# Performance work log

Hardware: AMD Instinct MI355X
Metric: run time of the kernel (lower is better)

Reference implementation:

```python
import jax, jax.numpy as jnp
import numpy as np

N_NODES = 100000


def gcn_conv(x, W, b, src, dst, n):
    """PyG GCNConv: add self-loops, symmetric normalization, aggregate."""
    x = x @ W  # [N, out]
    loop = jnp.arange(n, dtype=src.dtype)
    src_f = jnp.concatenate([src, loop])  # sources (message origins)
    dst_f = jnp.concatenate([dst, loop])  # targets (aggregation index)
    ones = jnp.ones(src_f.shape[0], dtype=x.dtype)
    deg = jax.ops.segment_sum(ones, dst_f, num_segments=n)
    dinv = jnp.where(deg > 0, jax.lax.rsqrt(deg), 0.0)
    norm = dinv[src_f] * dinv[dst_f]  # [E+N]
    msg = x[src_f] * norm[:, None]  # gather + scale
    out = jax.ops.segment_sum(msg, dst_f, num_segments=n)  # scatter-add
    return out + b


def setup_inputs() -> dict:
    key = jax.random.key(0)
    k1, k2, k3, k4 = jax.random.split(key, 4)
    in_f, hid, ncls = 128, 128, 64
    n_edges = 1600000
    x = jax.random.normal(k1, (N_NODES, in_f), dtype=jnp.float32)
    W1 = jax.random.normal(k2, (in_f, hid), dtype=jnp.float32) * (1.0 / np.sqrt(in_f))
    b1 = jnp.zeros((hid,), dtype=jnp.float32)
    W2 = jax.random.normal(k3, (hid, ncls), dtype=jnp.float32) * (1.0 / np.sqrt(hid))
    b2 = jnp.zeros((ncls,), dtype=jnp.float32)
    edge_index = jax.random.randint(k4, (2, n_edges), 0, N_NODES, dtype=jnp.int32)
    return {"x": x, "W1": W1, "b1": b1, "W2": W2, "b2": b2, "edge_index": edge_index}


def reference(x, W1, b1, W2, b2, edge_index):
    src, dst = edge_index[0], edge_index[1]
    n = x.shape[0]
    h = gcn_conv(x, W1, b1, src, dst, n)
    h = jax.nn.relu(h)
    # dropout p=0.5 is identity in eval mode
    h = gcn_conv(h, W2, b2, src, dst, n)
    return jax.nn.log_softmax(h, axis=1)
```

## Files before the change

kernel.cpp:

```cpp
#include <hip/hip_runtime.h>
#include <math.h>

#define N_NODES 100000
#define N_EDGES 1600000
#define NB 391
#define MROWS 100096
#define CH 3200

typedef __attribute__((ext_vector_type(8))) short short8;
typedef __attribute__((ext_vector_type(4))) float f32x4;
typedef __attribute__((ext_vector_type(2))) float f32x2;

__device__ __forceinline__ short f2b(float f) {
    unsigned u = __float_as_uint(f);
    unsigned r = (u + 0x7FFFu + ((u >> 16) & 1u)) >> 16;
    return (short)r;
}
__device__ __forceinline__ unsigned pk2(float a, float b) {
    return (unsigned)(unsigned short)f2b(a) | ((unsigned)(unsigned short)f2b(b) << 16);
}
__device__ __forceinline__ unsigned char f2q(float v) {
    return (unsigned char)(__builtin_amdgcn_cvt_pk_fp8_f32(v, 0.f, 0, false) & 0xFF);
}
__device__ __forceinline__ void acc2(f32x2* a, unsigned u) {
    a[0] += __builtin_amdgcn_cvt_pk_f32_fp8((int)u, false);
    a[1] += __builtin_amdgcn_cvt_pk_f32_fp8((int)u, true);
}
__device__ __forceinline__ void acc16(f32x2* a, uint4 u) {
    acc2(a + 0, u.x); acc2(a + 2, u.y); acc2(a + 4, u.z); acc2(a + 6, u.w);
}

__device__ __forceinline__ short8 pack8t(const float* __restrict__ p) {
    float4 v0 = ((const float4*)p)[0];
    float4 v1 = ((const float4*)p)[1];
    union { unsigned u[4]; short8 s; } r;
    r.u[0] = __builtin_amdgcn_perm(__float_as_uint(v0.y), __float_as_uint(v0.x), 0x07060302u);
    r.u[1] = __builtin_amdgcn_perm(__float_as_uint(v0.w), __float_as_uint(v0.z), 0x07060302u);
    r.u[2] = __builtin_amdgcn_perm(__float_as_uint(v1.y), __float_as_uint(v1.x), 0x07060302u);
    r.u[3] = __builtin_amdgcn_perm(__float_as_uint(v1.w), __float_as_uint(v1.z), 0x07060302u);
    return r.s;
}

__global__ __launch_bounds__(512) void init_misc(int* __restrict__ bcnt) {
    int t = threadIdx.x;
    if (t < NB) bcnt[t] = 0;
}

__global__ __launch_bounds__(256) void bucket_count(const int* __restrict__ dst,
                                                    int* __restrict__ bcnt) {
    __shared__ int h[NB];
    int t = threadIdx.x;
    for (int i = t; i < NB; i += 256) h[i] = 0;
    __syncthreads();
    for (int e = blockIdx.x * 256 + t; e < N_EDGES; e += gridDim.x * 256)
        atomicAdd(&h[dst[e] >> 8], 1);
    __syncthreads();
    for (int i = t; i < NB; i += 256)
        if (h[i]) atomicAdd(&bcnt[i], h[i]);
}

__global__ __launch_bounds__(512) void bucket_scan(const int* __restrict__ bcnt,
                                                   int* __restrict__ boffs,
                                                   int* __restrict__ bcur) {
    __shared__ int s[512];
    int t = threadIdx.x;
    int v = (t < NB) ? bcnt[t] : 0;
    s[t] = v;
    __syncthreads();
    for (int off = 1; off < 512; off <<= 1) {
        int u = (t >= off) ? s[t - off] : 0;
        __syncthreads();
        s[t] += u;
        __syncthreads();
    }
    if (t < NB) {
        int ex = s[t] - v;
        boffs[t] = ex;
        bcur[t] = ex;
    }
    if (t == 0) boffs[NB] = N_EDGES;
}

__global__ __launch_bounds__(256) void bucket_scatter(const int* __restrict__ src,
                                                      const int* __restrict__ dst,
                                                      int* __restrict__ bcur,
                                                      unsigned* __restrict__ pairs) {
    __shared__ unsigned lw[CH];
    __shared__ short lb[CH];
    __shared__ int cnt[NB];
    __shared__ int lstart[NB];
    int t = threadIdx.x;
    int e0 = blockIdx.x * CH;
    int n = min(CH, N_EDGES - e0);
    for (int i = t; i < NB; i += 256) cnt[i] = 0;
    __syncthreads();
    for (int i = t; i < n; i += 256) {
        int s = src[e0 + i], d = dst[e0 + i];
        lw[i] = ((unsigned)(d & 255) << 24) | (unsigned)s;
        int b = d >> 8;
        lb[i] = (short)b;
        atomicAdd(&cnt[b], 1);
    }
    __syncthreads();
    for (int b = t; b < NB; b += 256) {
        int c = cnt[b];
        lstart[b] = c ? atomicAdd(&bcur[b], c) : 0;
        cnt[b] = 0;
    }
    __syncthreads();
    for (int i = t; i < n; i += 256) {
        int b = lb[i];
        int lo = atomicAdd(&cnt[b], 1);
        pairs[lstart[b] + lo] = lw[i];
    }
}

__global__ __launch_bounds__(256) void csr_fill_bucket(const unsigned* __restrict__ pairs,
                                                       const int* __restrict__ boffs,
                                                       int2* __restrict__ rinfo,
                                                       float* __restrict__ dinv,
                                                       int* __restrict__ srcs) {
    __shared__ int lcnt[256];
    __shared__ int ls[256];
    int t = threadIdx.x, b = blockIdx.x, base = b << 8;
    lcnt[t] = 0;
    __syncthreads();
    int lo_e = boffs[b], hi_e = boffs[b + 1];
    for (int i = lo_e + t; i < hi_e; i += 256)
        atomicAdd(&lcnt[pairs[i] >> 24], 1);
    __syncthreads();
    int c = lcnt[t];
    int len = c + 1;
    ls[t] = len;
    __syncthreads();
    for (int off = 1; off < 256; off <<= 1) {
        int u = (t >= off) ? ls[t - off] : 0;
        __syncthreads();
        ls[t] += u;
        __syncthreads();
    }
    int rp = lo_e + base + ls[t] - len;
    int node = base + t;
    if (node < N_NODES) {
        rinfo[node] = make_int2(rp, rp + len);
        dinv[node] = rsqrtf((float)len);
        srcs[rp] = node;
    }
    __syncthreads();
    lcnt[t] = rp + 1;
    __syncthreads();
    for (int i = lo_e + t; i < hi_e; i += 256) {
        unsigned p = pairs[i];
        int li = p >> 24;
        int pos = atomicAdd(&lcnt[li], 1);
        srcs[pos] = (int)(p & 0xFFFFFFu);
    }
}

__global__ __launch_bounds__(256) void convert_w(const float* __restrict__ W1,
                                                 const float* __restrict__ W2,
                                                 short* __restrict__ w1h,
                                                 short* __restrict__ w2h) {
    int id = blockIdx.x * 256 + threadIdx.x;
    if (id < 128 * 128) {
        int n = id >> 7, k = id & 127;
        w1h[id] = f2b(W1[k * 128 + n]);
    } else if (id < 128 * 128 + 64 * 128) {
        int j = id - 128 * 128;
        int n = j >> 7, k = j & 127;
        w2h[j] = f2b(W2[k * 64 + n]);
    }
}

__global__ __launch_bounds__(512) void gemm1_mfma(const float* __restrict__ X,
                                                  const short* __restrict__ Wt,
                                                  const float* __restrict__ dinv,
                                                  unsigned char* __restrict__ Yf) {
    __shared__ short Ws[128 * 128];
    const int t = threadIdx.x;
    for (int i = t * 8; i < 128 * 128; i += 512 * 8)
        *(short8*)(Ws + i) = *(const short8*)(Wt + i);
    __syncthreads();

    const int w = t >> 6, lane = t & 63;
    const int m = lane & 15, q = lane >> 4;
    const int r0 = blockIdx.x * 128 + w * 16;
    const int ra = min(r0 + m, N_NODES - 1);

    f32x4 acc[8];
#pragma unroll
    for (int c = 0; c < 8; ++c) acc[c] = (f32x4)(0.f);

#pragma unroll
    for (int kk = 0; kk < 4; ++kk) {
        const int koff = kk * 32 + q * 8;
        short8 a = pack8t(X + (size_t)ra * 128 + koff);
#pragma unroll
        for (int c = 0; c < 8; ++c) {
            short8 bh = *(const short8*)(Ws + (c * 16 + m) * 128 + koff);
            acc[c] = __builtin_amdgcn_mfma_f32_16x16x32_bf16(a, bh, acc[c], 0, 0, 0);
        }
    }

    const int rb0 = r0 + q * 4;
    f32x4 dv = *(const f32x4*)(dinv + rb0);
#pragma unroll
    for (int c = 0; c < 8; ++c) {
        const int col = c * 16 + m;
#pragma unroll
        for (int r = 0; r < 4; ++r) {
            int row = rb0 + r;
            if (row < N_NODES) Yf[(size_t)row * 128 + col] = f2q(acc[c][r] * dv[r]);
        }
    }
}

__global__ __launch_bounds__(512) void gemm2_mfma(const short* __restrict__ H,
                                                  const short* __restrict__ Wt,
                                                  const float* __restrict__ dinv,
                                                  unsigned char* __restrict__ Yf) {
    __shared__ short Ws[64 * 128];
    const int t = threadIdx.x;
    for (int i = t * 8; i < 64 * 128; i += 512 * 8)
        *(short8*)(Ws + i) = *(const short8*)(Wt + i);
    __syncthreads();

    const int w = t >> 6, lane = t & 63;
    const int m = lane & 15, q = lane >> 4;
    const int r0 = blockIdx.x * 128 + w * 16;

    f32x4 acc[4];
#pragma unroll
    for (int c = 0; c < 4; ++c) acc[c] = (f32x4)(0.f);

#pragma unroll
    for (int kk = 0; kk < 4; ++kk) {
        const int koff = kk * 32 + q * 8;
        short8 a = *(const short8*)(H + (size_t)(r0 + m) * 128 + koff);
#pragma unroll
        for (int c = 0; c < 4; ++c) {
            short8 bh = *(const short8*)(Ws + (c * 16 + m) * 128 + koff);
            acc[c] = __builtin_amdgcn_mfma_f32_16x16x32_bf16(a, bh, acc[c], 0, 0, 0);
        }
    }

    const int rb0 = r0 + q * 4;
    f32x4 dv = *(const f32x4*)(dinv + rb0);
#pragma unroll
    for (int c = 0; c < 4; ++c) {
        const int col = c * 16 + m;
#pragma unroll
        for (int r = 0; r < 4; ++r) {
            int row = rb0 + r;
            if (row < N_NODES) Yf[(size_t)row * 64 + col] = f2q(acc[c][r] * dv[r]);
        }
    }
}

__global__ __launch_bounds__(256) void agg_relu(const int2* __restrict__ rinfo,
                                                const int* __restrict__ srcs,
                                                const unsigned char* __restrict__ Yf,
                                                const float* __restrict__ dinv,
                                                const float* __restrict__ b,
                                                short* __restrict__ Hb) {
    int t = threadIdx.x;
    int lane = t & 63, w = t >> 6;
    int g = lane >> 3, fl = lane & 7;
    int node = blockIdx.x * 32 + w * 8 + g;
    const unsigned fo = (unsigned)(fl << 4);
    int2 r = rinfo[node];
    int e = r.x, len = r.y - r.x;
    int mx = len;
    mx = max(mx, __shfl_xor(mx, 8));
    mx = max(mx, __shfl_xor(mx, 16));
    mx = max(mx, __shfl_xor(mx, 32));
    f32x2 a[8];
#pragma unroll
    for (int i = 0; i < 8; ++i) a[i] = (f32x2)(0.f);

    uint4 GA0, GA1;
    unsigned sB0 = 0, sB1 = 0;
    {
        unsigned s0 = (unsigned)srcs[e];
        GA0 = *(const uint4*)(Yf + ((s0 << 7) + fo));
        if (1 < len) {
            unsigned s1 = (unsigned)srcs[e + 1];
            GA1 = *(const uint4*)(Yf + ((s1 << 7) + fo));
        }
        if (2 < len) sB0 = (unsigned)srcs[e + 2];
        if (3 < len) sB1 = (unsigned)srcs[e + 3];
    }
    for (int i = 0; i < mx; i += 2) {
        uint4 GB0, GB1;
        if (i + 2 < len) GB0 = *(const uint4*)(Yf + ((sB0 << 7) + fo));
        if (i + 3 < len) GB1 = *(const uint4*)(Yf + ((sB1 << 7) + fo));
        unsigned sC0 = sB0, sC1 = sB1;
        if (i + 4 < len) sC0 = (unsigned)srcs[e + i + 4];
        if (i + 5 < len) sC1 = (unsigned)srcs[e + i + 5];
        if (i < len)     acc16(a, GA0);
        if (i + 1 < len) acc16(a, GA1);
        GA0 = GB0; GA1 = GB1; sB0 = sC0; sB1 = sC1;
    }

    float sc = dinv[node];
    const float4* bf = (const float4*)b;
    float bb[16];
    *(float4*)(bb + 0)  = bf[fl * 4 + 0];
    *(float4*)(bb + 4)  = bf[fl * 4 + 1];
    *(float4*)(bb + 8)  = bf[fl * 4 + 2];
    *(float4*)(bb + 12) = bf[fl * 4 + 3];
    unsigned u[8];
#pragma unroll
    for (int k = 0; k < 8; ++k) {
        float v0 = fmaxf(sc * a[k][0] + bb[2 * k], 0.f);
        float v1 = fmaxf(sc * a[k][1] + bb[2 * k + 1], 0.f);
        u[k] = pk2(v0, v1);
    }
    uint4* hp = (uint4*)Hb + (size_t)node * 16 + fl * 2;
    hp[0] = make_uint4(u[0], u[1], u[2], u[3]);
    hp[1] = make_uint4(u[4], u[5], u[6], u[7]);
}

__global__ __launch_bounds__(256) void agg_lsm(const int2* __restrict__ rinfo,
                                               const int* __restrict__ srcs,
                                               const unsigned char* __restrict__ Yf,
                                               const float* __restrict__ dinv,
                                               const float* __restrict__ b,
                                               float* __restrict__ out) {
    int t = threadIdx.x;
    int lane = t & 63, w = t >> 6;
    int g = lane >> 2, fl = lane & 3;
    int node = blockIdx.x * 64 + w * 16 + g;
    int nd = min(node, N_NODES - 1);
    const unsigned fo = (unsigned)(fl << 4);
    int2 r = rinfo[nd];
    int e = r.x, len = r.y - r.x;
    int mx = len;
    mx = max(mx, __shfl_xor(mx, 4));
    mx = max(mx, __shfl_xor(mx, 8));
    mx = max(mx, __shfl_xor(mx, 16));
    mx = max(mx, __shfl_xor(mx, 32));
    f32x2 a[8];
#pragma unroll
    for (int i = 0; i < 8; ++i) a[i] = (f32x2)(0.f);

    uint4 GA0, GA1;
    unsigned sB0 = 0, sB1 = 0;
    {
        unsigned s0 = (unsigned)srcs[e];
        GA0 = *(const uint4*)(Yf + ((s0 << 6) + fo));
        if (1 < len) {
            unsigned s1 = (unsigned)srcs[e + 1];
            GA1 = *(const uint4*)(Yf + ((s1 << 6) + fo));
        }
        if (2 < len) sB0 = (unsigned)srcs[e + 2];
        if (3 < len) sB1 = (unsigned)srcs[e + 3];
    }
    for (int i = 0; i < mx; i += 2) {
        uint4 GB0, GB1;
        if (i + 2 < len) GB0 = *(const uint4*)(Yf + ((sB0 << 6) + fo));
        if (i + 3 < len) GB1 = *(const uint4*)(Yf + ((sB1 << 6) + fo));
        unsigned sC0 = sB0, sC1 = sB1;
        if (i + 4 < len) sC0 = (unsigned)srcs[e + i + 4];
        if (i + 5 < len) sC1 = (unsigned)srcs[e + i + 5];
        if (i < len)     acc16(a, GA0);
        if (i + 1 < len) acc16(a, GA1);
        GA0 = GB0; GA1 = GB1; sB0 = sC0; sB1 = sC1;
    }

    float sc = dinv[nd];
    const float4* bf = (const float4*)b;
    float bb[16];
    *(float4*)(bb + 0)  = bf[fl * 4 + 0];
    *(float4*)(bb + 4)  = bf[fl * 4 + 1];
    *(float4*)(bb + 8)  = bf[fl * 4 + 2];
    *(float4*)(bb + 12) = bf[fl * 4 + 3];
    float v[16];
#pragma unroll
    for (int j = 0; j < 16; ++j) v[j] = sc * a[j >> 1][j & 1] + bb[j];
    float m = v[0];
#pragma unroll
    for (int j = 1; j < 16; ++j) m = fmaxf(m, v[j]);
    m = fmaxf(m, __shfl_xor(m, 1));
    m = fmaxf(m, __shfl_xor(m, 2));
    float su = 0.f;
#pragma unroll
    for (int j = 0; j < 16; ++j) su += __expf(v[j] - m);
    su += __shfl_xor(su, 1);
    su += __shfl_xor(su, 2);
    float ls = m + logf(su);
    if (node < N_NODES) {
        float4* op = (float4*)out + (size_t)node * 16 + fl * 4;
        op[0] = make_float4(v[0] - ls,  v[1] - ls,  v[2] - ls,  v[3] - ls);
        op[1] = make_float4(v[4] - ls,  v[5] - ls,  v[6] - ls,  v[7] - ls);
        op[2] = make_float4(v[8] - ls,  v[9] - ls,  v[10] - ls, v[11] - ls);
        op[3] = make_float4(v[12] - ls, v[13] - ls, v[14] - ls, v[15] - ls);
    }
}

extern "C" void kernel_launch(void* const* d_in, const int* in_sizes, int n_in,
                              void* d_out, int out_size, void* d_ws, size_t ws_size,
                              hipStream_t stream) {
    const float* x  = (const float*)d_in[0];
    const float* W1 = (const float*)d_in[1];
    const float* b1 = (const float*)d_in[2];
    const float* W2 = (const float*)d_in[3];
    const float* b2 = (const float*)d_in[4];
    const int* edge = (const int*)d_in[5];
    const int* src = edge;
    const int* dst = edge + N_EDGES;
    float* out = (float*)d_out;

    char* ws = (char*)d_ws;
    int*           bcnt  = (int*)(ws + 0);
    int*           boffs = (int*)(ws + 2048);
    int*           bcur  = (int*)(ws + 4096);
    float*         dinv  = (float*)(ws + 6144);
    int2*          rinfo = (int2*)(ws + 406528);
    int*           srcs  = (int*)(ws + 1206528);
    unsigned*      pairs = (unsigned*)(ws + 14012672);
    short*         w1h   = (short*)(ws + 20412672);
    short*         w2h   = (short*)(ws + 20445440);
    unsigned char* y1f   = (unsigned char*)(ws + 20461824);
    short*         h1b   = (short*)(ws + 33274112);
    unsigned char* y2f   = (unsigned char*)(ws + 58898688);

    init_misc<<<1, 512, 0, stream>>>(bcnt);

    bucket_count<<<512, 256, 0, stream>>>(dst, bcnt);
    bucket_scan<<<1, 512, 0, stream>>>(bcnt, boffs, bcur);
    bucket_scatter<<<(N_EDGES + CH - 1) / CH, 256, 0, stream>>>(src, dst, bcur, pairs);
    csr_fill_bucket<<<NB, 256, 0, stream>>>(pairs, boffs, rinfo, dinv, srcs);

    convert_w<<<(128 * 128 + 64 * 128 + 255) / 256, 256, 0, stream>>>(W1, W2, w1h, w2h);

    gemm1_mfma<<<MROWS / 128, 512, 0, stream>>>(x, w1h, dinv, y1f);
    agg_relu<<<N_NODES / 32, 256, 0, stream>>>(rinfo, srcs, y1f, dinv, b1, h1b);

    gemm2_mfma<<<MROWS / 128, 512, 0, stream>>>(h1b, w2h, dinv, y2f);
    agg_lsm<<<(N_NODES + 63) / 64, 256, 0, stream>>>(rinfo, srcs, y2f, dinv, b2, out);
}
```

Measured before the change: 257.9 us.

## Sort nodes by degree within buckets and deepen gather prefetch pipeline

During CSR construction each 256-node bucket builds a small degree histogram and writes a permutation that groups nodes of similar in-degree. The two aggregation kernels now process nodes in this order, so lanes in a wavefront have similar loop trip counts and less divergence. The gather loop is restructured to keep six rows in flight, with index loads issued a further six edges ahead, to hide memory latency. This adds an extra indirection load, scatters output writes across rows, and raises register pressure.

```diff
diff --git a/kernel.cpp b/kernel.cpp
--- a/kernel.cpp
+++ b/kernel.cpp
@@ -119,11 +119,15 @@
                                                        const int* __restrict__ boffs,
                                                        int2* __restrict__ rinfo,
                                                        float* __restrict__ dinv,
-                                                       int* __restrict__ srcs) {
+                                                       int* __restrict__ srcs,
+                                                       int* __restrict__ order) {
     __shared__ int lcnt[256];
     __shared__ int ls[256];
+    __shared__ int hist[64];
+    __shared__ int hoff[64];
     int t = threadIdx.x, b = blockIdx.x, base = b << 8;
     lcnt[t] = 0;
+    if (t < 64) hist[t] = 0;
     __syncthreads();
     int lo_e = boffs[b], hi_e = boffs[b + 1];
     for (int i = lo_e + t; i < hi_e; i += 256)
@@ -141,12 +145,22 @@
     }
     int rp = lo_e + base + ls[t] - len;
     int node = base + t;
-    if (node < N_NODES) {
+    bool valid = (node < N_NODES);
+    int bin = min(len, 63);
+    int sub = 0;
+    if (valid) {
         rinfo[node] = make_int2(rp, rp + len);
         dinv[node] = rsqrtf((float)len);
         srcs[rp] = node;
-    }
-    __syncthreads();
+        sub = atomicAdd(&hist[bin], 1);
+    }
+    __syncthreads();
+    if (t == 0) {
+        int a = 0;
+        for (int k = 0; k < 64; ++k) { hoff[k] = a; a += hist[k]; }
+    }
+    __syncthreads();
+    if (valid) order[base + hoff[bin] + sub] = node;
     lcnt[t] = rp + 1;
     __syncthreads();
     for (int i = lo_e + t; i < hi_e; i += 256) {
@@ -259,6 +273,7 @@
 
 __global__ __launch_bounds__(256) void agg_relu(const int2* __restrict__ rinfo,
                                                 const int* __restrict__ srcs,
+                                                const int* __restrict__ order,
                                                 const unsigned char* __restrict__ Yf,
                                                 const float* __restrict__ dinv,
                                                 const float* __restrict__ b,
@@ -266,7 +281,8 @@
     int t = threadIdx.x;
     int lane = t & 63, w = t >> 6;
     int g = lane >> 3, fl = lane & 7;
-    int node = blockIdx.x * 32 + w * 8 + g;
+    int slot = blockIdx.x * 32 + w * 8 + g;
+    int node = order[slot];
     const unsigned fo = (unsigned)(fl << 4);
     int2 r = rinfo[node];
     int e = r.x, len = r.y - r.x;
@@ -278,28 +294,41 @@
 #pragma unroll
     for (int i = 0; i < 8; ++i) a[i] = (f32x2)(0.f);
 
-    uint4 GA0, GA1;
-    unsigned sB0 = 0, sB1 = 0;
-    {
-        unsigned s0 = (unsigned)srcs[e];
-        GA0 = *(const uint4*)(Yf + ((s0 << 7) + fo));
-        if (1 < len) {
-            unsigned s1 = (unsigned)srcs[e + 1];
-            GA1 = *(const uint4*)(Yf + ((s1 << 7) + fo));
-        }
-        if (2 < len) sB0 = (unsigned)srcs[e + 2];
-        if (3 < len) sB1 = (unsigned)srcs[e + 3];
-    }
-    for (int i = 0; i < mx; i += 2) {
-        uint4 GB0, GB1;
-        if (i + 2 < len) GB0 = *(const uint4*)(Yf + ((sB0 << 7) + fo));
-        if (i + 3 < len) GB1 = *(const uint4*)(Yf + ((sB1 << 7) + fo));
-        unsigned sC0 = sB0, sC1 = sB1;
-        if (i + 4 < len) sC0 = (unsigned)srcs[e + i + 4];
-        if (i + 5 < len) sC1 = (unsigned)srcs[e + i + 5];
-        if (i < len)     acc16(a, GA0);
-        if (i + 1 < len) acc16(a, GA1);
-        GA0 = GB0; GA1 = GB1; sB0 = sC0; sB1 = sC1;
+    auto ld = [&](int i) -> unsigned {
+        unsigned v = 0;
+        if (i < len) v = (unsigned)srcs[e + i];
+        return v;
+    };
+    auto gth = [&](unsigned s) -> uint4 {
+        return *(const uint4*)(Yf + ((s << 7) + fo));
+    };
+
+    unsigned sA0 = ld(0), sA1 = ld(1), sB0 = ld(2), sB1 = ld(3), sC0 = ld(4), sC1 = ld(5);
+    uint4 GA0, GA1, GB0, GB1, GC0, GC1;
+    if (0 < len) GA0 = gth(sA0);
+    if (1 < len) GA1 = gth(sA1);
+    if (2 < len) GB0 = gth(sB0);
+    if (3 < len) GB1 = gth(sB1);
+    if (4 < len) GC0 = gth(sC0);
+    if (5 < len) GC1 = gth(sC1);
+    sA0 = ld(6); sA1 = ld(7); sB0 = ld(8); sB1 = ld(9); sC0 = ld(10); sC1 = ld(11);
+
+    for (int i = 0; i < mx; i += 6) {
+        if (i < len)      acc16(a, GA0);
+        if (i + 1 < len)  acc16(a, GA1);
+        if (i + 6 < len)  GA0 = gth(sA0);
+        if (i + 7 < len)  GA1 = gth(sA1);
+        if (i + 2 < len)  acc16(a, GB0);
+        if (i + 3 < len)  acc16(a, GB1);
+        if (i + 8 < len)  GB0 = gth(sB0);
+        if (i + 9 < len)  GB1 = gth(sB1);
+        if (i + 4 < len)  acc16(a, GC0);
+        if (i + 5 < len)  acc16(a, GC1);
+        if (i + 10 < len) GC0 = gth(sC0);
+        if (i + 11 < len) GC1 = gth(sC1);
+        sA0 = ld(i + 12); sA1 = ld(i + 13);
+        sB0 = ld(i + 14); sB1 = ld(i + 15);
+        sC0 = ld(i + 16); sC1 = ld(i + 17);
     }
 
     float sc = dinv[node];
@@ -323,6 +352,7 @@
 
 __global__ __launch_bounds__(256) void agg_lsm(const int2* __restrict__ rinfo,
                                                const int* __restrict__ srcs,
+                                               const int* __restrict__ order,
                                                const unsigned char* __restrict__ Yf,
                                                const float* __restrict__ dinv,
                                                const float* __restrict__ b,
@@ -330,10 +360,10 @@
     int t = threadIdx.x;
     int lane = t & 63, w = t >> 6;
     int g = lane >> 2, fl = lane & 3;
-    int node = blockIdx.x * 64 + w * 16 + g;
-    int nd = min(node, N_NODES - 1);
+    int slot = blockIdx.x * 64 + w * 16 + g;
+    int node = order[min(slot, N_NODES - 1)];
     const unsigned fo = (unsigned)(fl << 4);
-    int2 r = rinfo[nd];
+    int2 r = rinfo[node];
     int e = r.x, len = r.y - r.x;
     int mx = len;
     mx = max(mx, __shfl_xor(mx, 4));
@@ -344,31 +374,44 @@
 #pragma unroll
     for (int i = 0; i < 8; ++i) a[i] = (f32x2)(0.f);
 
-    uint4 GA0, GA1;
-    unsigned sB0 = 0, sB1 = 0;
-    {
-        unsigned s0 = (unsigned)srcs[e];
-        GA0 = *(const uint4*)(Yf + ((s0 << 6) + fo));
-        if (1 < len) {
-            unsigned s1 = (unsigned)srcs[e + 1];
-            GA1 = *(const uint4*)(Yf + ((s1 << 6) + fo));
-        }
-        if (2 < len) sB0 = (unsigned)srcs[e + 2];
-        if (3 < len) sB1 = (unsigned)srcs[e + 3];
-    }
-    for (int i = 0; i < mx; i += 2) {
-        uint4 GB0, GB1;
-        if (i + 2 < len) GB0 = *(const uint4*)(Yf + ((sB0 << 6) + fo));
-        if (i + 3 < len) GB1 = *(const uint4*)(Yf + ((sB1 << 6) + fo));
-        unsigned sC0 = sB0, sC1 = sB1;
-        if (i + 4 < len) sC0 = (unsigned)srcs[e + i + 4];
-        if (i + 5 < len) sC1 = (unsigned)srcs[e + i + 5];
-        if (i < len)     acc16(a, GA0);
-        if (i + 1 < len) acc16(a, GA1);
-        GA0 = GB0; GA1 = GB1; sB0 = sC0; sB1 = sC1;
-    }
-
-    float sc = dinv[nd];
+    auto ld = [&](int i) -> unsigned {
+        unsigned v = 0;
+        if (i < len) v = (unsigned)srcs[e + i];
+        return v;
+    };
+    auto gth = [&](unsigned s) -> uint4 {
+        return *(const uint4*)(Yf + ((s << 6) + fo));
+    };
+
+    unsigned sA0 = ld(0), sA1 = ld(1), sB0 = ld(2), sB1 = ld(3), sC0 = ld(4), sC1 = ld(5);
+    uint4 GA0, GA1, GB0, GB1, GC0, GC1;
+    if (0 < len) GA0 = gth(sA0);
+    if (1 < len) GA1 = gth(sA1);
+    if (2 < len) GB0 = gth(sB0);
+    if (3 < len) GB1 = gth(sB1);
+    if (4 < len) GC0 = gth(sC0);
+    if (5 < len) GC1 = gth(sC1);
+    sA0 = ld(6); sA1 = ld(7); sB0 = ld(8); sB1 = ld(9); sC0 = ld(10); sC1 = ld(11);
+
+    for (int i = 0; i < mx; i += 6) {
+        if (i < len)      acc16(a, GA0);
+        if (i + 1 < len)  acc16(a, GA1);
+        if (i + 6 < len)  GA0 = gth(sA0);
+        if (i + 7 < len)  GA1 = gth(sA1);
+        if (i + 2 < len)  acc16(a, GB0);
+        if (i + 3 < len)  acc16(a, GB1);
+        if (i + 8 < len)  GB0 = gth(sB0);
+        if (i + 9 < len)  GB1 = gth(sB1);
+        if (i + 4 < len)  acc16(a, GC0);
+        if (i + 5 < len)  acc16(a, GC1);
+        if (i + 10 < len) GC0 = gth(sC0);
+        if (i + 11 < len) GC1 = gth(sC1);
+        sA0 = ld(i + 12); sA1 = ld(i + 13);
+        sB0 = ld(i + 14); sB1 = ld(i + 15);
+        sC0 = ld(i + 16); sC1 = ld(i + 17);
+    }
+
+    float sc = dinv[node];
     const float4* bf = (const float4*)b;
     float bb[16];
     *(float4*)(bb + 0)  = bf[fl * 4 + 0];
@@ -389,7 +432,7 @@
     su += __shfl_xor(su, 1);
     su += __shfl_xor(su, 2);
     float ls = m + logf(su);
-    if (node < N_NODES) {
+    if (slot < N_NODES) {
         float4* op = (float4*)out + (size_t)node * 16 + fl * 4;
         op[0] = make_float4(v[0] - ls,  v[1] - ls,  v[2] - ls,  v[3] - ls);
         op[1] = make_float4(v[4] - ls,  v[5] - ls,  v[6] - ls,  v[7] - ls);
@@ -418,6 +461,7 @@
     float*         dinv  = (float*)(ws + 6144);
     int2*          rinfo = (int2*)(ws + 406528);
     int*           srcs  = (int*)(ws + 1206528);
+    int*           order = (int*)(ws + 8106560);
     unsigned*      pairs = (unsigned*)(ws + 14012672);
     short*         w1h   = (short*)(ws + 20412672);
     short*         w2h   = (short*)(ws + 20445440);
@@ -430,13 +474,13 @@
     bucket_count<<<512, 256, 0, stream>>>(dst, bcnt);
     bucket_scan<<<1, 512, 0, stream>>>(bcnt, boffs, bcur);
     bucket_scatter<<<(N_EDGES + CH - 1) / CH, 256, 0, stream>>>(src, dst, bcur, pairs);
-    csr_fill_bucket<<<NB, 256, 0, stream>>>(pairs, boffs, rinfo, dinv, srcs);
+    csr_fill_bucket<<<NB, 256, 0, stream>>>(pairs, boffs, rinfo, dinv, srcs, order);
 
     convert_w<<<(128 * 128 + 64 * 128 + 255) / 256, 256, 0, stream>>>(W1, W2, w1h, w2h);
 
     gemm1_mfma<<<MROWS / 128, 512, 0, stream>>>(x, w1h, dinv, y1f);
-    agg_relu<<<N_NODES / 32, 256, 0, stream>>>(rinfo, srcs, y1f, dinv, b1, h1b);
+    agg_relu<<<N_NODES / 32, 256, 0, stream>>>(rinfo, srcs, order, y1f, dinv, b1, h1b);
 
     gemm2_mfma<<<MROWS / 128, 512, 0, stream>>>(h1b, w2h, dinv, y2f);
-    agg_lsm<<<(N_NODES + 63) / 64, 256, 0, stream>>>(rinfo, srcs, y2f, dinv, b2, out);
-}
+    agg_lsm<<<(N_NODES + 63) / 64, 256, 0, stream>>>(rinfo, srcs, order, y2f, dinv, b2, out);
+}
```

Result: slower. 280.9 us (+8.9%).

## Sort nodes by degree within buckets to balance aggregation wavefronts

Applied to the files above, without the earlier changes.

csr_fill_bucket now builds a per-bucket counting sort of nodes by in-degree (capped at 63) and writes a permutation array. Both aggregation kernels read node ids through this permutation and map waves across blocks so that each wavefront handles nodes of similar degree. This is meant to cut divergence, where a wave loops up to the max degree of its nodes. The cost is an extra indirection load, scattered output writes, and a serial prefix over 64 bins in the fill kernel.

```diff
diff --git a/kernel.cpp b/kernel.cpp
--- a/kernel.cpp
+++ b/kernel.cpp
@@ -119,11 +119,15 @@
                                                        const int* __restrict__ boffs,
                                                        int2* __restrict__ rinfo,
                                                        float* __restrict__ dinv,
-                                                       int* __restrict__ srcs) {
+                                                       int* __restrict__ srcs,
+                                                       int* __restrict__ order) {
     __shared__ int lcnt[256];
     __shared__ int ls[256];
+    __shared__ int hist[64];
+    __shared__ int hoff[64];
     int t = threadIdx.x, b = blockIdx.x, base = b << 8;
     lcnt[t] = 0;
+    if (t < 64) hist[t] = 0;
     __syncthreads();
     int lo_e = boffs[b], hi_e = boffs[b + 1];
     for (int i = lo_e + t; i < hi_e; i += 256)
@@ -141,12 +145,22 @@
     }
     int rp = lo_e + base + ls[t] - len;
     int node = base + t;
-    if (node < N_NODES) {
+    bool valid = (node < N_NODES);
+    int bin = min(len, 63);
+    int sub = 0;
+    if (valid) {
         rinfo[node] = make_int2(rp, rp + len);
         dinv[node] = rsqrtf((float)len);
         srcs[rp] = node;
-    }
-    __syncthreads();
+        sub = atomicAdd(&hist[bin], 1);
+    }
+    __syncthreads();
+    if (t == 0) {
+        int a = 0;
+        for (int k = 0; k < 64; ++k) { hoff[k] = a; a += hist[k]; }
+    }
+    __syncthreads();
+    if (valid) order[base + hoff[bin] + sub] = node;
     lcnt[t] = rp + 1;
     __syncthreads();
     for (int i = lo_e + t; i < hi_e; i += 256) {
@@ -259,6 +273,7 @@
 
 __global__ __launch_bounds__(256) void agg_relu(const int2* __restrict__ rinfo,
                                                 const int* __restrict__ srcs,
+                                                const int* __restrict__ order,
                                                 const unsigned char* __restrict__ Yf,
                                                 const float* __restrict__ dinv,
                                                 const float* __restrict__ b,
@@ -266,7 +281,12 @@
     int t = threadIdx.x;
     int lane = t & 63, w = t >> 6;
     int g = lane >> 3, fl = lane & 7;
-    int node = blockIdx.x * 32 + w * 8 + g;
+    int bucket = blockIdx.x >> 3;
+    int ib = blockIdx.x & 7;
+    int j = (bucket == NB - 1) ? (ib * 4 + w)
+                               : (w * 8 + ib);
+    int slot = (bucket << 8) + j * 8 + g;
+    int node = order[slot];
     const unsigned fo = (unsigned)(fl << 4);
     int2 r = rinfo[node];
     int e = r.x, len = r.y - r.x;
@@ -323,6 +343,7 @@
 
 __global__ __launch_bounds__(256) void agg_lsm(const int2* __restrict__ rinfo,
                                                const int* __restrict__ srcs,
+                                               const int* __restrict__ order,
                                                const unsigned char* __restrict__ Yf,
                                                const float* __restrict__ dinv,
                                                const float* __restrict__ b,
@@ -330,10 +351,16 @@
     int t = threadIdx.x;
     int lane = t & 63, w = t >> 6;
     int g = lane >> 2, fl = lane & 3;
-    int node = blockIdx.x * 64 + w * 16 + g;
-    int nd = min(node, N_NODES - 1);
+    int bucket = blockIdx.x >> 2;
+    int ib = blockIdx.x & 3;
+    bool lastb = (bucket == NB - 1);
+    int j = lastb ? (ib * 4 + w) : (w * 4 + ib);
+    int bn = lastb ? (N_NODES - ((NB - 1) << 8)) : 256;
+    int sl = j * 16 + g;
+    int slot = (bucket << 8) + min(sl, bn - 1);
+    int node = order[slot];
     const unsigned fo = (unsigned)(fl << 4);
-    int2 r = rinfo[nd];
+    int2 r = rinfo[node];
     int e = r.x, len = r.y - r.x;
     int mx = len;
     mx = max(mx, __shfl_xor(mx, 4));
@@ -368,7 +395,7 @@
         GA0 = GB0; GA1 = GB1; sB0 = sC0; sB1 = sC1;
     }
 
-    float sc = dinv[nd];
+    float sc = dinv[node];
     const float4* bf = (const float4*)b;
     float bb[16];
     *(float4*)(bb + 0)  = bf[fl * 4 + 0];
@@ -377,19 +404,19 @@
     *(float4*)(bb + 12) = bf[fl * 4 + 3];
     float v[16];
 #pragma unroll
-    for (int j = 0; j < 16; ++j) v[j] = sc * a[j >> 1][j & 1] + bb[j];
+    for (int j2 = 0; j2 < 16; ++j2) v[j2] = sc * a[j2 >> 1][j2 & 1] + bb[j2];
     float m = v[0];
 #pragma unroll
-    for (int j = 1; j < 16; ++j) m = fmaxf(m, v[j]);
+    for (int j2 = 1; j2 < 16; ++j2) m = fmaxf(m, v[j2]);
     m = fmaxf(m, __shfl_xor(m, 1));
     m = fmaxf(m, __shfl_xor(m, 2));
     float su = 0.f;
 #pragma unroll
-    for (int j = 0; j < 16; ++j) su += __expf(v[j] - m);
+    for (int j2 = 0; j2 < 16; ++j2) su += __expf(v[j2] - m);
     su += __shfl_xor(su, 1);
     su += __shfl_xor(su, 2);
     float ls = m + logf(su);
-    if (node < N_NODES) {
+    if (sl < bn) {
         float4* op = (float4*)out + (size_t)node * 16 + fl * 4;
         op[0] = make_float4(v[0] - ls,  v[1] - ls,  v[2] - ls,  v[3] - ls);
         op[1] = make_float4(v[4] - ls,  v[5] - ls,  v[6] - ls,  v[7] - ls);
@@ -418,6 +445,7 @@
     float*         dinv  = (float*)(ws + 6144);
     int2*          rinfo = (int2*)(ws + 406528);
     int*           srcs  = (int*)(ws + 1206528);
+    int*           order = (int*)(ws + 8106560);
     unsigned*      pairs = (unsigned*)(ws + 14012672);
     short*         w1h   = (short*)(ws + 20412672);
     short*         w2h   = (short*)(ws + 20445440);
@@ -430,13 +458,13 @@
     bucket_count<<<512, 256, 0, stream>>>(dst, bcnt);
     bucket_scan<<<1, 512, 0, stream>>>(bcnt, boffs, bcur);
     bucket_scatter<<<(N_EDGES + CH - 1) / CH, 256, 0, stream>>>(src, dst, bcur, pairs);
-    csr_fill_bucket<<<NB, 256, 0, stream>>>(pairs, boffs, rinfo, dinv, srcs);
+    csr_fill_bucket<<<NB, 256, 0, stream>>>(pairs, boffs, rinfo, dinv, srcs, order);
 
     convert_w<<<(128 * 128 + 64 * 128 + 255) / 256, 256, 0, stream>>>(W1, W2, w1h, w2h);
 
     gemm1_mfma<<<MROWS / 128, 512, 0, stream>>>(x, w1h, dinv, y1f);
-    agg_relu<<<N_NODES / 32, 256, 0, stream>>>(rinfo, srcs, y1f, dinv, b1, h1b);
+    agg_relu<<<N_NODES / 32, 256, 0, stream>>>(rinfo, srcs, order, y1f, dinv, b1, h1b);
 
     gemm2_mfma<<<MROWS / 128, 512, 0, stream>>>(h1b, w2h, dinv, y2f);
-    agg_lsm<<<(N_NODES + 63) / 64, 256, 0, stream>>>(rinfo, srcs, y2f, dinv, b2, out);
-}
+    agg_lsm<<<(N_NODES + 63) / 64, 256, 0, stream>>>(rinfo, srcs, order, y2f, dinv, b2, out);
+}
```

After: 267.7 us. 1.04x slower.

## Split layer-1 features into column chunks for cache-resident aggregation gather

Applied to the files above, without the earlier changes.

gemm1 now writes its fp8 output as four column-chunked planes of 32 bytes per node instead of interleaved 128-byte rows. agg_relu is relaunched with 512-thread blocks, each handling a 256-node bucket for one 32-column chunk. Each gather therefore touches a 3.2MB plane that can stay resident in L2/LLC. The cost is that the CSR source indices are re-read four times, and each lane gathers only 16 bytes per edge.

```diff
diff --git a/kernel.cpp b/kernel.cpp
--- a/kernel.cpp
+++ b/kernel.cpp
@@ -206,11 +206,11 @@
     f32x4 dv = *(const f32x4*)(dinv + rb0);
 #pragma unroll
     for (int c = 0; c < 8; ++c) {
-        const int col = c * 16 + m;
+        const size_t coff = ((size_t)(c >> 1) * MROWS) * 32 + (c & 1) * 16 + m;
 #pragma unroll
         for (int r = 0; r < 4; ++r) {
             int row = rb0 + r;
-            if (row < N_NODES) Yf[(size_t)row * 128 + col] = f2q(acc[c][r] * dv[r]);
+            if (row < N_NODES) Yf[coff + (size_t)row * 32] = f2q(acc[c][r] * dv[r]);
         }
     }
 }
@@ -257,20 +257,29 @@
     }
 }
 
-__global__ __launch_bounds__(256) void agg_relu(const int2* __restrict__ rinfo,
+__global__ __launch_bounds__(512) void agg_relu(const int2* __restrict__ rinfo,
                                                 const int* __restrict__ srcs,
-                                                const unsigned char* __restrict__ Yf,
+                                                const unsigned char* __restrict__ Yc,
                                                 const float* __restrict__ dinv,
                                                 const float* __restrict__ b,
                                                 short* __restrict__ Hb) {
     int t = threadIdx.x;
     int lane = t & 63, w = t >> 6;
-    int g = lane >> 3, fl = lane & 7;
-    int node = blockIdx.x * 32 + w * 8 + g;
+    int x = blockIdx.x & 7;
+    int q = blockIdx.x >> 3;
+    int c = x >> 1;
+    int bucket = q * 2 + (x & 1);
+    if (bucket >= NB) return;
+    int g = lane >> 1, fl = lane & 1;
+    int node = (bucket << 8) + w * 32 + g;
+    int nd = min(node, N_NODES - 1);
+    const unsigned char* Yb = Yc + (size_t)c * MROWS * 32;
     const unsigned fo = (unsigned)(fl << 4);
-    int2 r = rinfo[node];
+    int2 r = rinfo[nd];
     int e = r.x, len = r.y - r.x;
     int mx = len;
+    mx = max(mx, __shfl_xor(mx, 2));
+    mx = max(mx, __shfl_xor(mx, 4));
     mx = max(mx, __shfl_xor(mx, 8));
     mx = max(mx, __shfl_xor(mx, 16));
     mx = max(mx, __shfl_xor(mx, 32));
@@ -282,18 +291,18 @@
     unsigned sB0 = 0, sB1 = 0;
     {
         unsigned s0 = (unsigned)srcs[e];
-        GA0 = *(const uint4*)(Yf + ((s0 << 7) + fo));
+        GA0 = *(const uint4*)(Yb + ((size_t)s0 << 5) + fo);
         if (1 < len) {
             unsigned s1 = (unsigned)srcs[e + 1];
-            GA1 = *(const uint4*)(Yf + ((s1 << 7) + fo));
+            GA1 = *(const uint4*)(Yb + ((size_t)s1 << 5) + fo);
         }
         if (2 < len) sB0 = (unsigned)srcs[e + 2];
         if (3 < len) sB1 = (unsigned)srcs[e + 3];
     }
     for (int i = 0; i < mx; i += 2) {
         uint4 GB0, GB1;
-        if (i + 2 < len) GB0 = *(const uint4*)(Yf + ((sB0 << 7) + fo));
-        if (i + 3 < len) GB1 = *(const uint4*)(Yf + ((sB1 << 7) + fo));
+        if (i + 2 < len) GB0 = *(const uint4*)(Yb + ((size_t)sB0 << 5) + fo);
+        if (i + 3 < len) GB1 = *(const uint4*)(Yb + ((size_t)sB1 << 5) + fo);
         unsigned sC0 = sB0, sC1 = sB1;
         if (i + 4 < len) sC0 = (unsigned)srcs[e + i + 4];
         if (i + 5 < len) sC1 = (unsigned)srcs[e + i + 5];
@@ -302,13 +311,13 @@
         GA0 = GB0; GA1 = GB1; sB0 = sC0; sB1 = sC1;
     }
 
-    float sc = dinv[node];
-    const float4* bf = (const float4*)b;
+    float sc = dinv[nd];
+    const float4* bf = (const float4*)(b + c * 32 + fl * 16);
     float bb[16];
-    *(float4*)(bb + 0)  = bf[fl * 4 + 0];
-    *(float4*)(bb + 4)  = bf[fl * 4 + 1];
-    *(float4*)(bb + 8)  = bf[fl * 4 + 2];
-    *(float4*)(bb + 12) = bf[fl * 4 + 3];
+    *(float4*)(bb + 0)  = bf[0];
+    *(float4*)(bb + 4)  = bf[1];
+    *(float4*)(bb + 8)  = bf[2];
+    *(float4*)(bb + 12) = bf[3];
     unsigned u[8];
 #pragma unroll
     for (int k = 0; k < 8; ++k) {
@@ -316,9 +325,11 @@
         float v1 = fmaxf(sc * a[k][1] + bb[2 * k + 1], 0.f);
         u[k] = pk2(v0, v1);
     }
-    uint4* hp = (uint4*)Hb + (size_t)node * 16 + fl * 2;
-    hp[0] = make_uint4(u[0], u[1], u[2], u[3]);
-    hp[1] = make_uint4(u[4], u[5], u[6], u[7]);
+    if (node < N_NODES) {
+        uint4* hp = (uint4*)((char*)Hb + ((size_t)node << 8) + (c << 6) + (fl << 5));
+        hp[0] = make_uint4(u[0], u[1], u[2], u[3]);
+        hp[1] = make_uint4(u[4], u[5], u[6], u[7]);
+    }
 }
 
 __global__ __launch_bounds__(256) void agg_lsm(const int2* __restrict__ rinfo,
@@ -435,7 +446,7 @@
     convert_w<<<(128 * 128 + 64 * 128 + 255) / 256, 256, 0, stream>>>(W1, W2, w1h, w2h);
 
     gemm1_mfma<<<MROWS / 128, 512, 0, stream>>>(x, w1h, dinv, y1f);
-    agg_relu<<<N_NODES / 32, 256, 0, stream>>>(rinfo, srcs, y1f, dinv, b1, h1b);
+    agg_relu<<<196 * 8, 512, 0, stream>>>(rinfo, srcs, y1f, dinv, b1, h1b);
 
     gemm2_mfma<<<MROWS / 128, 512, 0, stream>>>(h1b, w2h, dinv, y2f);
     agg_lsm<<<(N_NODES + 63) / 64, 256, 0, stream>>>(rinfo, srcs, y2f, dinv, b2, out);
```

New measurement: 291.4 us. +13.0%, slower.
